# Optimization experiments

Measured on AMD Instinct MI355X. Metric: run time of the kernel, lower is better.

The kernel has to match this reference:

```python
import jax, jax.numpy as jnp
import numpy as np

N = 4096
D = 1024

def setup_inputs() -> dict:
    key = jax.random.key(0)
    k1, k2, k3, k4, k5, k6 = jax.random.split(key, 6)
    x_l = jax.random.normal(k1, (1, N, D), dtype=jnp.float32)
    x_r = jax.random.normal(k2, (1, N, D), dtype=jnp.float32)
    # mask encodes: (u,v) in legal_pairs AND locator[u,v] endpoints not in bucket
    mask = jax.random.randint(k3, (N, N), 0, 2) > 0
    # xavier_uniform for bilinear matrix
    limit = float(np.sqrt(6.0 / (D + D)))
    matrix = jax.random.uniform(k4, (D, D), dtype=jnp.float32, minval=-limit, maxval=limit)
    bias = jnp.zeros((1,), dtype=jnp.float32)
    wl = jax.random.normal(k5, (1, D), dtype=jnp.float32) * 0.02
    bl = jnp.zeros((1,), dtype=jnp.float32)
    wr = jax.random.normal(k6, (1, D), dtype=jnp.float32) * 0.02
    br = jnp.zeros((1,), dtype=jnp.float32)
    return {"x_l": x_l, "x_r": x_r, "mask": mask, "matrix": matrix,
            "bias": bias, "wl": wl, "bl": bl, "wr": wr, "br": br, "s_ind": 0}

def reference(x_l, x_r, mask, matrix, bias, wl, bl, wr, br, s_ind):
    # biaffine: x_l @ M @ x_r^T + bias  -> [1, n, n]
    xm = jnp.einsum('bnl,lr->bnr', x_l, matrix)
    x = jnp.einsum('bnr,bmr->bnm', xm, x_r) + bias[0]
    # linear terms: lin_l(x_l) -> [1,n,1]; lin_r(x_r)^T -> [1,1,n]
    lin_l = jnp.einsum('bnl,ol->bno', x_l, wl) + bl  # [1, n, 1]
    lin_r = jnp.einsum('bnr,or->bno', x_r, wr) + br  # [1, n, 1]
    x = x + lin_l + jnp.swapaxes(lin_r, 1, 2)
    x = jax.nn.relu(x)
    x = x[0]  # squeeze batch -> [n, n]
    # vectorized form of the legal_pairs / hypergraph-bucket scatter loop
    scores = jnp.where(mask, x, jnp.zeros((), dtype=x.dtype))
    return (scores, x)
```

## Files before the change

kernel.cpp:

```cpp
#include <hip/hip_runtime.h>
#include <stdint.h>
#include <stddef.h>

#define NTOK 4096
#define DDIM 1024

typedef __attribute__((ext_vector_type(4))) float f32x4;
typedef __attribute__((ext_vector_type(8))) short s16x8;
typedef __attribute__((ext_vector_type(4))) unsigned short u16x4;
typedef __attribute__((ext_vector_type(4))) int i32x4;

__device__ __forceinline__ unsigned short f2bf(float f) {
  union { float f; unsigned u; } v; v.f = f;
  unsigned u = v.u + 0x7fffu + ((v.u >> 16) & 1u);
  return (unsigned short)(u >> 16);
}

__device__ __forceinline__ void gload_lds16(const void* g, void* l) {
  __builtin_amdgcn_global_load_lds(
      (const __attribute__((address_space(1))) void*)g,
      (__attribute__((address_space(3))) void*)l, 16, 0, 0);
}

#define VMWAIT(N) asm volatile("s_waitcnt vmcnt(" #N ")" ::: "memory")

__global__ void convlin_k(const float* __restrict__ x, const float* __restrict__ w,
                          const float* __restrict__ b0, const float* __restrict__ b1,
                          unsigned short* __restrict__ xb, float* __restrict__ lin) {
  int wv = threadIdx.x >> 6, lane = threadIdx.x & 63;
  int row = blockIdx.x * 4 + wv;
  const f32x4* xr = (const f32x4*)(x + (size_t)row * DDIM);
  const f32x4* w4 = (const f32x4*)w;
  u16x4* xb4 = (u16x4*)(xb + (size_t)row * DDIM);
  float s = 0.f;
  for (int j = lane; j < DDIM / 4; j += 64) {
    f32x4 a = xr[j], c = w4[j];
    s += a[0] * c[0] + a[1] * c[1] + a[2] * c[2] + a[3] * c[3];
    u16x4 o;
    o[0] = f2bf(a[0]); o[1] = f2bf(a[1]); o[2] = f2bf(a[2]); o[3] = f2bf(a[3]);
    xb4[j] = o;
  }
#pragma unroll
  for (int off = 32; off; off >>= 1) s += __shfl_down(s, off);
  if (lane == 0) lin[row] = s + b0[0] + (b1 ? b1[0] : 0.f);
}

__global__ void transpose_bf16_k(const float* __restrict__ M,
                                 unsigned short* __restrict__ Mt) {
  __shared__ unsigned short tile[32][33];
  int tx = threadIdx.x, ty = threadIdx.y;
  int bx = blockIdx.x, by = blockIdx.y;
  int x = bx * 32 + tx;
  for (int i = ty; i < 32; i += 8)
    tile[i][tx] = f2bf(M[(size_t)(by * 32 + i) * DDIM + x]);
  __syncthreads();
  int ox = by * 32 + tx;
  for (int i = ty; i < 32; i += 8)
    Mt[(size_t)(bx * 32 + i) * DDIM + ox] = tile[tx][i];
}

__global__ void detect_mask_k(const unsigned char* __restrict__ m, int* __restrict__ flag) {
  __shared__ int f;
  if (threadIdx.x == 0) f = 0;
  __syncthreads();
  int any = 0;
  for (int i = threadIdx.x; i < 4096; i += 256)
    if ((i & 3) && m[i]) any = 1;
  if (any) atomicOr(&f, 1);
  __syncthreads();
  if (threadIdx.x == 0) *flag = f;
}

__launch_bounds__(512, 4)
__global__ void gemm1_k(const unsigned short* __restrict__ A,
                        const unsigned short* __restrict__ B,
                        unsigned short* __restrict__ Cb) {
  constexpr int BM = 64, BN = 128, K = DDIM;
  constexpr int MF = 2, NF = 2, AI = 1, BI = 2;
  __shared__ unsigned short As[2][BM][64];
  __shared__ unsigned short Bs[2][BN][64];

  const int lin = blockIdx.x;
  const int cpx = gridDim.x >> 3;
  const int swz = (lin & 7) * cpx + (lin >> 3);
  const int bi = swz >> 3, bj = swz & 7;

  const int tid = threadIdx.x;
  const int wid = tid >> 6, lane = tid & 63;
  const int wr2 = wid >> 2, wc2 = wid & 3;
  const int l15 = lane & 15, l16 = lane >> 4;
  const int xm = lane & 7;

  const int srow0 = tid >> 3;
  const int swslot = (tid & 7) ^ (srow0 & 7);
  const unsigned short* Ag = A + (size_t)(bi * BM + srow0) * K + swslot * 8;
  const unsigned short* Bg = B + (size_t)(bj * BN + srow0) * K + swslot * 8;

  f32x4 acc[MF][NF] = {};

#define STAGE_G1(BUF, K0)                                                    \
  {                                                                          \
    _Pragma("unroll") for (int j = 0; j < AI; ++j)                           \
        gload_lds16(Ag + (size_t)(j * 64) * K + (K0),                        \
                    &As[BUF][0][0] + j * 4096 + wid * 512);                  \
    _Pragma("unroll") for (int j = 0; j < BI; ++j)                           \
        gload_lds16(Bg + (size_t)(j * 64) * K + (K0),                        \
                    &Bs[BUF][0][0] + j * 4096 + wid * 512);                  \
  }

  STAGE_G1(0, 0)
  VMWAIT(0);
  __builtin_amdgcn_s_barrier();

  for (int t = 0; t < 16; ++t) {
    const int cur = t & 1, nxt = cur ^ 1;
    if (t < 15) STAGE_G1(nxt, (t + 1) * 64)
#pragma unroll
    for (int kk = 0; kk < 2; ++kk) {
      s16x8 Areg[MF], Breg[NF];
#pragma unroll
      for (int m = 0; m < MF; ++m)
        Areg[m] = *(const s16x8*)&As[cur][wr2 * 32 + m * 16 + l15]
                                     [(((kk << 2) | l16) ^ xm) << 3];
#pragma unroll
      for (int n = 0; n < NF; ++n)
        Breg[n] = *(const s16x8*)&Bs[cur][wc2 * 32 + n * 16 + l15]
                                     [(((kk << 2) | l16) ^ xm) << 3];
      __builtin_amdgcn_s_setprio(1);
#pragma unroll
      for (int m = 0; m < MF; ++m)
#pragma unroll
        for (int n = 0; n < NF; ++n)
          acc[m][n] = __builtin_amdgcn_mfma_f32_16x16x32_bf16(
              Areg[m], Breg[n], acc[m][n], 0, 0, 0);
      __builtin_amdgcn_s_setprio(0);
    }
    VMWAIT(0);
    __builtin_amdgcn_s_barrier();
  }
#undef STAGE_G1

#pragma unroll
  for (int m = 0; m < MF; ++m) {
    int row0 = bi * BM + wr2 * 32 + m * 16 + 4 * l16;
#pragma unroll
    for (int n = 0; n < NF; ++n) {
      int col = bj * BN + wc2 * 32 + n * 16 + l15;
#pragma unroll
      for (int r = 0; r < 4; ++r)
        Cb[(size_t)(row0 + r) * DDIM + col] = f2bf(acc[m][n][r]);
    }
  }
}

__launch_bounds__(512, 2)
__global__ void gemm2_k(const unsigned short* __restrict__ A,
                        const unsigned short* __restrict__ B,
                        const float* __restrict__ linl,
                        const float* __restrict__ linr,
                        const void* __restrict__ mask,
                        const int* __restrict__ mflag,
                        float* __restrict__ scores,
                        float* __restrict__ xout) {
  constexpr int K = DDIM;
  __shared__ __align__(16) unsigned char smem[147456];
  unsigned short* sA = (unsigned short*)smem;
  unsigned short* sB = sA + 3 * 16384;

  const int lin = blockIdx.x;
  const int xcd = lin & 7, w = lin >> 3;
  const int bi = (xcd & 1) * 8 + (w >> 3);
  const int bj = (xcd >> 1) * 8 + (w & 7);

  const int tid = threadIdx.x;
  const int wid = tid >> 6, lane = tid & 63;
  const int wm = wid >> 1, wn = wid & 1;
  const int l15 = lane & 15, l16 = lane >> 4;
  const int xm = lane & 7;

  const int srow0 = tid >> 3;
  const int swslot = (tid & 7) ^ (srow0 & 7);
  const unsigned short* Ag = A + (size_t)(bi * 256 + srow0) * K + swslot * 8;
  const unsigned short* Bg = B + (size_t)(bj * 128 + srow0) * K + swslot * 8;

  f32x4 acc[4][4] = {};

#define STG_A(BUF, K0)                                                       \
  {                                                                          \
    _Pragma("unroll") for (int j = 0; j < 4; ++j)                            \
        gload_lds16(Ag + (size_t)(j * 64) * K + (K0),                        \
                    sA + (BUF)*16384 + j * 4096 + wid * 512);                \
  }
#define STG_B(BUF, K0)                                                       \
  {                                                                          \
    _Pragma("unroll") for (int j = 0; j < 2; ++j)                            \
        gload_lds16(Bg + (size_t)(j * 64) * K + (K0),                        \
                    sB + (BUF)*8192 + j * 4096 + wid * 512);                 \
  }

  STG_A(0, 0) STG_B(0, 0)
  STG_A(1, 64) STG_B(1, 64)
  VMWAIT(6);
  __builtin_amdgcn_s_barrier();

  int cb = 0;
  for (int t = 0; t < 16; ++t) {
    const int sb = (cb + 2 >= 3) ? cb - 1 : cb + 2;
    const unsigned short* As0 = sA + cb * 16384;
    const unsigned short* Bs0 = sB + cb * 8192;
#pragma unroll
    for (int kk = 0; kk < 2; ++kk) {
      s16x8 Areg[4], Breg[4];
#pragma unroll
      for (int m = 0; m < 4; ++m)
        Areg[m] = *(const s16x8*)(As0 + (wm * 64 + m * 16 + l15) * 64 +
                                  ((((kk << 2) | l16) ^ xm) << 3));
#pragma unroll
      for (int n = 0; n < 4; ++n)
        Breg[n] = *(const s16x8*)(Bs0 + (wn * 64 + n * 16 + l15) * 64 +
                                  ((((kk << 2) | l16) ^ xm) << 3));
      if (t < 14) {
        if (kk == 0) { STG_A(sb, (t + 2) * 64) }
        else         { STG_B(sb, (t + 2) * 64) }
      }
      __builtin_amdgcn_s_setprio(1);
#pragma unroll
      for (int m = 0; m < 4; ++m)
#pragma unroll
        for (int n = 0; n < 4; ++n)
          acc[m][n] = __builtin_amdgcn_mfma_f32_16x16x32_bf16(
              Areg[m], Breg[n], acc[m][n], 0, 0, 0);
      __builtin_amdgcn_s_setprio(0);
    }
    if (t < 14) { VMWAIT(6); }
    else if (t == 14) { VMWAIT(0); }
    if (t < 15) __builtin_amdgcn_s_barrier();
    cb = (cb + 1 == 3) ? 0 : cb + 1;
  }
#undef STG_A
#undef STG_B

  __syncthreads();
  float* Cf = (float*)smem;
#pragma unroll
  for (int m = 0; m < 4; ++m) {
#pragma unroll
    for (int n = 0; n < 4; ++n) {
      int lc = wn * 64 + n * 16 + l15;
#pragma unroll
      for (int r = 0; r < 4; ++r) {
        int lr = wm * 64 + m * 16 + l16 * 4 + r;
        Cf[lr * 128 + (lc ^ (((lr >> 2) & 1) << 4))] = acc[m][n][r];
      }
    }
  }
  __syncthreads();

  const int mf = *mflag;
#pragma unroll
  for (int it = 0; it < 16; ++it) {
    int fid = it * 512 + tid;
    int lr = fid >> 5, sl = fid & 31;
    int c0 = sl << 2;
    int cs = c0 ^ (((lr >> 2) & 1) << 4);
    f32x4 v4 = *(const f32x4*)&Cf[lr * 128 + cs];
    int row = bi * 256 + lr;
    int colb = bj * 128 + c0;
    float ll = linl[row];
    f32x4 rr = *(const f32x4*)&linr[colb];
    size_t idx = (size_t)row * NTOK + colb;
    f32x4 o, sc;
    if (mf) {
      unsigned m4 = *(const unsigned*)((const unsigned char*)mask + idx);
#pragma unroll
      for (int e = 0; e < 4; ++e) {
        float v = v4[e] + ll + rr[e];
        v = v > 0.f ? v : 0.f;
        o[e] = v; sc[e] = ((m4 >> (8 * e)) & 255u) ? v : 0.f;
      }
    } else {
      i32x4 m4 = *(const i32x4*)((const int*)mask + idx);
#pragma unroll
      for (int e = 0; e < 4; ++e) {
        float v = v4[e] + ll + rr[e];
        v = v > 0.f ? v : 0.f;
        o[e] = v; sc[e] = m4[e] ? v : 0.f;
      }
    }
    *(f32x4*)&xout[idx] = o;
    *(f32x4*)&scores[idx] = sc;
  }
}

extern "C" void kernel_launch(void* const* d_in, const int* in_sizes, int n_in,
                              void* d_out, int out_size, void* d_ws, size_t ws_size,
                              hipStream_t stream) {
  const float* x_l    = (const float*)d_in[0];
  const float* x_r    = (const float*)d_in[1];
  const void*  maskp  = (const void*)d_in[2];
  const float* matrix = (const float*)d_in[3];
  const float* bias   = (const float*)d_in[4];
  const float* wl     = (const float*)d_in[5];
  const float* bl     = (const float*)d_in[6];
  const float* wr     = (const float*)d_in[7];
  const float* br     = (const float*)d_in[8];

  unsigned short* XLb = (unsigned short*)d_ws;
  unsigned short* XRb = XLb + (size_t)NTOK * DDIM;
  unsigned short* XMb = XRb + (size_t)NTOK * DDIM;
  unsigned short* Mtb = XMb + (size_t)NTOK * DDIM;
  float* lin_l = (float*)(Mtb + (size_t)DDIM * DDIM);
  float* lin_r = lin_l + NTOK;
  int* mflag = (int*)(lin_r + NTOK);

  float* scores = (float*)d_out;
  float* xout = scores + (size_t)NTOK * NTOK;

  convlin_k<<<NTOK / 4, 256, 0, stream>>>(x_l, wl, bl, bias, XLb, lin_l);
  convlin_k<<<NTOK / 4, 256, 0, stream>>>(x_r, wr, br, nullptr, XRb, lin_r);
  transpose_bf16_k<<<dim3(32, 32), dim3(32, 8), 0, stream>>>(matrix, Mtb);
  detect_mask_k<<<1, 256, 0, stream>>>((const unsigned char*)maskp, mflag);

  gemm1_k<<<512, 512, 0, stream>>>(XLb, Mtb, XMb);

  gemm2_k<<<512, 512, 0, stream>>>(XMb, XRb, lin_l, lin_r, maskp, mflag,
                                   scores, xout);
}
```

Before: 111.2 us.

## Retile second GEMM to 128x128 tiles with a 5-stage, K=32 LDS pipeline

The fused biaffine GEMM+epilogue kernel moves from 256x128 output tiles with a 3-buffer, K=64 pipeline to 128x128 tiles with a 5-buffer, K=32 pipeline. LDS use drops from 144KB to 80KB and the grid doubles to 1024 blocks, with a new block-to-tile mapping grouped by XCD. The launch bound is raised to 4 blocks per CU. The aim is higher occupancy, so the memory-bound masked epilogue stores overlap better with MFMA work from other blocks. The cost is more reloading of A/B tiles and a tighter register budget that could cause spills.

```diff
diff --git a/kernel.cpp b/kernel.cpp
--- a/kernel.cpp
+++ b/kernel.cpp
@@ -153,7 +153,7 @@
   }
 }
 
-__launch_bounds__(512, 2)
+__launch_bounds__(512, 4)
 __global__ void gemm2_k(const unsigned short* __restrict__ A,
                         const unsigned short* __restrict__ B,
                         const float* __restrict__ linl,
@@ -163,93 +163,89 @@
                         float* __restrict__ scores,
                         float* __restrict__ xout) {
   constexpr int K = DDIM;
-  __shared__ __align__(16) unsigned char smem[147456];
-  unsigned short* sA = (unsigned short*)smem;
-  unsigned short* sB = sA + 3 * 16384;
+  __shared__ __align__(16) unsigned short sAB[5 * 4096 * 2];
+  unsigned short* sA = sAB;
+  unsigned short* sB = sAB + 5 * 4096;
 
   const int lin = blockIdx.x;
-  const int xcd = lin & 7, w = lin >> 3;
-  const int bi = (xcd & 1) * 8 + (w >> 3);
-  const int bj = (xcd >> 1) * 8 + (w & 7);
+  const int xcd = lin & 7, s = lin >> 3;
+  const int p = (s >> 5) * 8 + xcd;
+  const int w = s & 31;
+  const int bi = (p >> 2) * 4 + (w >> 3);
+  const int bj = (p & 3) * 8 + (w & 7);
 
   const int tid = threadIdx.x;
   const int wid = tid >> 6, lane = tid & 63;
-  const int wm = wid >> 1, wn = wid & 1;
+  const int wr2 = wid >> 2, wc2 = wid & 3;
   const int l15 = lane & 15, l16 = lane >> 4;
-  const int xm = lane & 7;
-
-  const int srow0 = tid >> 3;
-  const int swslot = (tid & 7) ^ (srow0 & 7);
-  const unsigned short* Ag = A + (size_t)(bi * 256 + srow0) * K + swslot * 8;
+  const int xs = (l15 >> 1) & 3;
+
+  const int srow0 = tid >> 2;
+  const int swslot = (tid & 3) ^ ((srow0 >> 1) & 3);
+  const unsigned short* Ag = A + (size_t)(bi * 128 + srow0) * K + swslot * 8;
   const unsigned short* Bg = B + (size_t)(bj * 128 + srow0) * K + swslot * 8;
 
-  f32x4 acc[4][4] = {};
-
-#define STG_A(BUF, K0)                                                       \
+  f32x4 acc[4][2] = {};
+
+#define STG2(BUF, K0)                                                        \
   {                                                                          \
-    _Pragma("unroll") for (int j = 0; j < 4; ++j)                            \
-        gload_lds16(Ag + (size_t)(j * 64) * K + (K0),                        \
-                    sA + (BUF)*16384 + j * 4096 + wid * 512);                \
-  }
-#define STG_B(BUF, K0)                                                       \
+    gload_lds16(Ag + (K0), sA + (BUF)*4096 + wid * 512);                     \
+    gload_lds16(Bg + (K0), sB + (BUF)*4096 + wid * 512);                     \
+  }
+
+#define T_BODY(DOSTG, K0S, WAITSTMT, DOBAR)                                  \
   {                                                                          \
-    _Pragma("unroll") for (int j = 0; j < 2; ++j)                            \
-        gload_lds16(Bg + (size_t)(j * 64) * K + (K0),                        \
-                    sB + (BUF)*8192 + j * 4096 + wid * 512);                 \
-  }
-
-  STG_A(0, 0) STG_B(0, 0)
-  STG_A(1, 64) STG_B(1, 64)
+    const unsigned short* As0 = sA + cb * 4096;                              \
+    const unsigned short* Bs0 = sB + cb * 4096;                              \
+    s16x8 Areg[4], Breg[2];                                                  \
+    _Pragma("unroll") for (int m = 0; m < 4; ++m)                            \
+        Areg[m] = *(const s16x8*)(As0 + (wr2 * 64 + m * 16 + l15) * 32 +     \
+                                  ((l16 ^ xs) << 3));                        \
+    _Pragma("unroll") for (int n = 0; n < 2; ++n)                            \
+        Breg[n] = *(const s16x8*)(Bs0 + (wc2 * 32 + n * 16 + l15) * 32 +     \
+                                  ((l16 ^ xs) << 3));                        \
+    if (DOSTG) { STG2(sb, K0S) }                                             \
+    __builtin_amdgcn_s_setprio(1);                                           \
+    _Pragma("unroll") for (int m = 0; m < 4; ++m)                            \
+        _Pragma("unroll") for (int n = 0; n < 2; ++n)                        \
+            acc[m][n] = __builtin_amdgcn_mfma_f32_16x16x32_bf16(             \
+                Areg[m], Breg[n], acc[m][n], 0, 0, 0);                       \
+    __builtin_amdgcn_s_setprio(0);                                           \
+    WAITSTMT                                                                 \
+    if (DOBAR) __builtin_amdgcn_s_barrier();                                 \
+    cb = (cb + 1 == 5) ? 0 : cb + 1;                                         \
+  }
+
+  STG2(0, 0) STG2(1, 32) STG2(2, 64) STG2(3, 96)
   VMWAIT(6);
   __builtin_amdgcn_s_barrier();
 
   int cb = 0;
-  for (int t = 0; t < 16; ++t) {
-    const int sb = (cb + 2 >= 3) ? cb - 1 : cb + 2;
-    const unsigned short* As0 = sA + cb * 16384;
-    const unsigned short* Bs0 = sB + cb * 8192;
-#pragma unroll
-    for (int kk = 0; kk < 2; ++kk) {
-      s16x8 Areg[4], Breg[4];
-#pragma unroll
-      for (int m = 0; m < 4; ++m)
-        Areg[m] = *(const s16x8*)(As0 + (wm * 64 + m * 16 + l15) * 64 +
-                                  ((((kk << 2) | l16) ^ xm) << 3));
-#pragma unroll
-      for (int n = 0; n < 4; ++n)
-        Breg[n] = *(const s16x8*)(Bs0 + (wn * 64 + n * 16 + l15) * 64 +
-                                  ((((kk << 2) | l16) ^ xm) << 3));
-      if (t < 14) {
-        if (kk == 0) { STG_A(sb, (t + 2) * 64) }
-        else         { STG_B(sb, (t + 2) * 64) }
-      }
-      __builtin_amdgcn_s_setprio(1);
-#pragma unroll
-      for (int m = 0; m < 4; ++m)
-#pragma unroll
-        for (int n = 0; n < 4; ++n)
-          acc[m][n] = __builtin_amdgcn_mfma_f32_16x16x32_bf16(
-              Areg[m], Breg[n], acc[m][n], 0, 0, 0);
-      __builtin_amdgcn_s_setprio(0);
-    }
-    if (t < 14) { VMWAIT(6); }
-    else if (t == 14) { VMWAIT(0); }
-    if (t < 15) __builtin_amdgcn_s_barrier();
-    cb = (cb + 1 == 3) ? 0 : cb + 1;
-  }
-#undef STG_A
-#undef STG_B
-
-  __syncthreads();
-  float* Cf = (float*)smem;
+  for (int t = 0; t < 28; ++t) {
+    const int sb = cb ? cb - 1 : 4;
+    T_BODY(1, (t + 4) * 32, VMWAIT(6);, 1)
+  }
+  {
+    const int sb = 0;
+    (void)sb;
+    T_BODY(0, 0, VMWAIT(4);, 1)
+    T_BODY(0, 0, VMWAIT(2);, 1)
+    T_BODY(0, 0, VMWAIT(0);, 1)
+    T_BODY(0, 0, , 0)
+  }
+#undef T_BODY
+#undef STG2
+
+  __syncthreads();
+  float* Cf = (float*)sAB;
 #pragma unroll
   for (int m = 0; m < 4; ++m) {
 #pragma unroll
-    for (int n = 0; n < 4; ++n) {
-      int lc = wn * 64 + n * 16 + l15;
+    for (int n = 0; n < 2; ++n) {
+      int lc = wc2 * 32 + n * 16 + l15;
 #pragma unroll
       for (int r = 0; r < 4; ++r) {
-        int lr = wm * 64 + m * 16 + l16 * 4 + r;
+        int lr = wr2 * 64 + m * 16 + l16 * 4 + r;
         Cf[lr * 128 + (lc ^ (((lr >> 2) & 1) << 4))] = acc[m][n][r];
       }
     }
@@ -258,13 +254,13 @@
 
   const int mf = *mflag;
 #pragma unroll
-  for (int it = 0; it < 16; ++it) {
+  for (int it = 0; it < 8; ++it) {
     int fid = it * 512 + tid;
     int lr = fid >> 5, sl = fid & 31;
     int c0 = sl << 2;
     int cs = c0 ^ (((lr >> 2) & 1) << 4);
     f32x4 v4 = *(const f32x4*)&Cf[lr * 128 + cs];
-    int row = bi * 256 + lr;
+    int row = bi * 128 + lr;
     int colb = bj * 128 + c0;
     float ll = linl[row];
     f32x4 rr = *(const f32x4*)&linr[colb];
@@ -323,6 +319,6 @@
 
   gemm1_k<<<512, 512, 0, stream>>>(XLb, Mtb, XMb);
 
-  gemm2_k<<<512, 512, 0, stream>>>(XMb, XRb, lin_l, lin_r, maskp, mflag,
-                                   scores, xout);
-}
+  gemm2_k<<<1024, 512, 0, stream>>>(XMb, XRb, lin_l, lin_r, maskp, mflag,
+                                    scores, xout);
+}
```

After: 94.24 us. 15.3% less time.

## Shrink gemm2 tiles to 128x128 with 256 threads and double buffering

Applied to the files above, without the earlier changes.

The second GEMM moves from 256x128 tiles with 512 threads and a triple-buffered LDS pipeline to 128x128 tiles with 256 threads, a smaller double-buffered LDS footprint, and 1024 blocks with a new XCD-aware block mapping. Smaller LDS use is meant to let more blocks be resident per CU and to give a finer grid. In exchange, operand reuse per block drops, more global traffic is needed, and the prefetch distance shrinks from two stages to one with a full vmcnt(0) wait each iteration.

```diff
diff --git a/kernel.cpp b/kernel.cpp
--- a/kernel.cpp
+++ b/kernel.cpp
@@ -153,7 +153,7 @@
   }
 }
 
-__launch_bounds__(512, 2)
+__launch_bounds__(256, 2)
 __global__ void gemm2_k(const unsigned short* __restrict__ A,
                         const unsigned short* __restrict__ B,
                         const float* __restrict__ linl,
@@ -163,66 +163,60 @@
                         float* __restrict__ scores,
                         float* __restrict__ xout) {
   constexpr int K = DDIM;
-  __shared__ __align__(16) unsigned char smem[147456];
-  unsigned short* sA = (unsigned short*)smem;
-  unsigned short* sB = sA + 3 * 16384;
+  __shared__ __align__(16) unsigned short sAB[4 * 8192];
+  unsigned short* sA = sAB;
+  unsigned short* sB = sAB + 2 * 8192;
 
   const int lin = blockIdx.x;
-  const int xcd = lin & 7, w = lin >> 3;
-  const int bi = (xcd & 1) * 8 + (w >> 3);
-  const int bj = (xcd >> 1) * 8 + (w & 7);
+  const int xcd = lin & 7, s = lin >> 3;
+  const int p = (s >> 5) * 8 + xcd;
+  const int w = s & 31;
+  const int bi = (p >> 2) * 4 + (w >> 3);
+  const int bj = (p & 3) * 8 + (w & 7);
 
   const int tid = threadIdx.x;
   const int wid = tid >> 6, lane = tid & 63;
-  const int wm = wid >> 1, wn = wid & 1;
+  const int wr2 = wid >> 1, wc2 = wid & 1;
   const int l15 = lane & 15, l16 = lane >> 4;
   const int xm = lane & 7;
 
   const int srow0 = tid >> 3;
   const int swslot = (tid & 7) ^ (srow0 & 7);
-  const unsigned short* Ag = A + (size_t)(bi * 256 + srow0) * K + swslot * 8;
+  const unsigned short* Ag = A + (size_t)(bi * 128 + srow0) * K + swslot * 8;
   const unsigned short* Bg = B + (size_t)(bj * 128 + srow0) * K + swslot * 8;
 
   f32x4 acc[4][4] = {};
 
-#define STG_A(BUF, K0)                                                       \
+#define STG2(BUF, K0)                                                        \
   {                                                                          \
-    _Pragma("unroll") for (int j = 0; j < 4; ++j)                            \
-        gload_lds16(Ag + (size_t)(j * 64) * K + (K0),                        \
-                    sA + (BUF)*16384 + j * 4096 + wid * 512);                \
-  }
-#define STG_B(BUF, K0)                                                       \
-  {                                                                          \
-    _Pragma("unroll") for (int j = 0; j < 2; ++j)                            \
-        gload_lds16(Bg + (size_t)(j * 64) * K + (K0),                        \
-                    sB + (BUF)*8192 + j * 4096 + wid * 512);                 \
-  }
-
-  STG_A(0, 0) STG_B(0, 0)
-  STG_A(1, 64) STG_B(1, 64)
-  VMWAIT(6);
+    _Pragma("unroll") for (int j = 0; j < 4; ++j) {                          \
+      gload_lds16(Ag + (size_t)(j * 32) * K + (K0),                          \
+                  sA + (BUF)*8192 + j * 2048 + wid * 512);                   \
+      gload_lds16(Bg + (size_t)(j * 32) * K + (K0),                          \
+                  sB + (BUF)*8192 + j * 2048 + wid * 512);                   \
+    }                                                                        \
+  }
+
+  STG2(0, 0)
+  VMWAIT(0);
   __builtin_amdgcn_s_barrier();
 
-  int cb = 0;
   for (int t = 0; t < 16; ++t) {
-    const int sb = (cb + 2 >= 3) ? cb - 1 : cb + 2;
-    const unsigned short* As0 = sA + cb * 16384;
-    const unsigned short* Bs0 = sB + cb * 8192;
+    const int cur = t & 1, nxt = cur ^ 1;
+    if (t < 15) STG2(nxt, (t + 1) * 64)
 #pragma unroll
     for (int kk = 0; kk < 2; ++kk) {
       s16x8 Areg[4], Breg[4];
 #pragma unroll
       for (int m = 0; m < 4; ++m)
-        Areg[m] = *(const s16x8*)(As0 + (wm * 64 + m * 16 + l15) * 64 +
+        Areg[m] = *(const s16x8*)(sA + cur * 8192 +
+                                  (wr2 * 64 + m * 16 + l15) * 64 +
                                   ((((kk << 2) | l16) ^ xm) << 3));
 #pragma unroll
       for (int n = 0; n < 4; ++n)
-        Breg[n] = *(const s16x8*)(Bs0 + (wn * 64 + n * 16 + l15) * 64 +
+        Breg[n] = *(const s16x8*)(sB + cur * 8192 +
+                                  (wc2 * 64 + n * 16 + l15) * 64 +
                                   ((((kk << 2) | l16) ^ xm) << 3));
-      if (t < 14) {
-        if (kk == 0) { STG_A(sb, (t + 2) * 64) }
-        else         { STG_B(sb, (t + 2) * 64) }
-      }
       __builtin_amdgcn_s_setprio(1);
 #pragma unroll
       for (int m = 0; m < 4; ++m)
@@ -232,24 +226,21 @@
               Areg[m], Breg[n], acc[m][n], 0, 0, 0);
       __builtin_amdgcn_s_setprio(0);
     }
-    if (t < 14) { VMWAIT(6); }
-    else if (t == 14) { VMWAIT(0); }
-    if (t < 15) __builtin_amdgcn_s_barrier();
-    cb = (cb + 1 == 3) ? 0 : cb + 1;
-  }
-#undef STG_A
-#undef STG_B
-
-  __syncthreads();
-  float* Cf = (float*)smem;
+    VMWAIT(0);
+    __builtin_amdgcn_s_barrier();
+  }
+#undef STG2
+
+  __syncthreads();
+  float* Cf = (float*)sAB;
 #pragma unroll
   for (int m = 0; m < 4; ++m) {
 #pragma unroll
     for (int n = 0; n < 4; ++n) {
-      int lc = wn * 64 + n * 16 + l15;
+      int lc = wc2 * 64 + n * 16 + l15;
 #pragma unroll
       for (int r = 0; r < 4; ++r) {
-        int lr = wm * 64 + m * 16 + l16 * 4 + r;
+        int lr = wr2 * 64 + m * 16 + l16 * 4 + r;
         Cf[lr * 128 + (lc ^ (((lr >> 2) & 1) << 4))] = acc[m][n][r];
       }
     }
@@ -259,12 +250,12 @@
   const int mf = *mflag;
 #pragma unroll
   for (int it = 0; it < 16; ++it) {
-    int fid = it * 512 + tid;
+    int fid = it * 256 + tid;
     int lr = fid >> 5, sl = fid & 31;
     int c0 = sl << 2;
     int cs = c0 ^ (((lr >> 2) & 1) << 4);
     f32x4 v4 = *(const f32x4*)&Cf[lr * 128 + cs];
-    int row = bi * 256 + lr;
+    int row = bi * 128 + lr;
     int colb = bj * 128 + c0;
     float ll = linl[row];
     f32x4 rr = *(const f32x4*)&linr[colb];
@@ -323,6 +314,6 @@
 
   gemm1_k<<<512, 512, 0, stream>>>(XLb, Mtb, XMb);
 
-  gemm2_k<<<512, 512, 0, stream>>>(XMb, XRb, lin_l, lin_r, maskp, mflag,
-                                   scores, xout);
-}
+  gemm2_k<<<1024, 256, 0, stream>>>(XMb, XRb, lin_l, lin_r, maskp, mflag,
+                                    scores, xout);
+}
```

Result: faster. 108.2 us (-2.7%).
